# Kernel optimization log

Hardware: AMD Instinct MI355X
Metric: run time of the kernel (lower is better)

Reference implementation:

```python
import jax, jax.numpy as jnp
import numpy as np

B, S, HID = 2, 2048, 1024
NH, HD = 16, 64  # op_heads, head_size; op_size = NH*HD = 1024


def setup_inputs() -> dict:
    key = jax.random.key(0)
    k1, k2, k3 = jax.random.split(key, 3)
    hidden_states = jax.random.normal(k1, (B, S, HID), dtype=jnp.float32)
    # Linear weights stored as [in, out] for x @ W + b
    Wqk = jax.random.normal(k2, (HID, 2 * NH * HD), dtype=jnp.float32) * (HID ** -0.5)
    bqk = jnp.zeros((2 * NH * HD,), dtype=jnp.float32)
    Wv = jax.random.normal(k3, (HID, NH * HD), dtype=jnp.float32) * (HID ** -0.5)
    bv = jnp.zeros((NH * HD,), dtype=jnp.float32)
    return {"hidden_states": hidden_states, "Wqk": Wqk, "bqk": bqk, "Wv": Wv, "bv": bv}


def _split_heads(t):
    # [B, S, NH*HD] -> [B, NH, S, HD]
    b, s, _ = t.shape
    return t.reshape(b, s, NH, HD).transpose(0, 2, 1, 3)


def reference(hidden_states, Wqk, bqk, Wv, bv):
    op_size = NH * HD
    qk = hidden_states @ Wqk + bqk                      # [B, S, 2*op_size]
    query, key = qk[..., :op_size], qk[..., op_size:]
    value = hidden_states @ Wv + bv                     # [B, S, op_size]
    q = _split_heads(query)                             # [B, H, S, D]
    k = _split_heads(key)
    v = _split_heads(value)
    # scores: [B, H, Sq, Sk], scaled by sqrt(head_dim) (scale_attn_weights=True)
    scores = jnp.einsum('bhqd,bhkd->bhqk', q, k) / jnp.asarray(HD ** 0.5, q.dtype)
    s = scores.shape[-1]
    causal = jnp.tril(jnp.ones((s, s), dtype=bool))     # [S, S]
    mask_value = jnp.finfo(scores.dtype).min
    scores = jnp.where(causal, scores, mask_value)
    attn = jax.nn.softmax(scores, axis=-1)              # dropout is identity (eval)
    out = jnp.einsum('bhqk,bhkd->bhqd', attn, v)        # [B, H, S, D]
    out = out.transpose(0, 2, 1, 3).reshape(out.shape[0], out.shape[2], NH * HD)
    return out
```

## Files before the change

kernel.cpp:

```cpp
#include <hip/hip_runtime.h>

typedef float floatx4 __attribute__((ext_vector_type(4)));
typedef float floatx16 __attribute__((ext_vector_type(16)));
typedef __bf16 bf16x8 __attribute__((ext_vector_type(8)));
typedef unsigned short u16x8 __attribute__((ext_vector_type(8)));
typedef unsigned short u16x4 __attribute__((ext_vector_type(4)));

#define GLDS16(g, l) __builtin_amdgcn_global_load_lds( \
    (__attribute__((address_space(1))) void*)(g), \
    (__attribute__((address_space(3))) void*)(l), 16, 0, 0)

__device__ __forceinline__ unsigned short f2bf(float f) {
    unsigned u = __float_as_uint(f);
    u += 0x7fffu + ((u >> 16) & 1u);
    return (unsigned short)(u >> 16);
}

#if __has_builtin(__builtin_amdgcn_cvt_pk_bf16_f32)
__device__ __forceinline__ unsigned pk2(float a, float b) {
    typedef __bf16 bf16x2 __attribute__((ext_vector_type(2)));
    union { bf16x2 v; unsigned u; } cv;
    cv.v = __builtin_amdgcn_cvt_pk_bf16_f32(a, b);
    return cv.u;
}
#else
__device__ __forceinline__ unsigned pk2(float a, float b) {
    return (unsigned)f2bf(a) | ((unsigned)f2bf(b) << 16);
}
#endif

#if __has_builtin(__builtin_amdgcn_exp2f)
__device__ __forceinline__ float fast_exp2(float x) { return __builtin_amdgcn_exp2f(x); }
#else
__device__ __forceinline__ float fast_exp2(float x) { return __exp2f(x); }
#endif

__global__ __launch_bounds__(256) void k_prep(const float* __restrict__ hidden,
                                              const float* __restrict__ Wqk,
                                              const float* __restrict__ Wv,
                                              unsigned short* __restrict__ Abf,
                                              unsigned short* __restrict__ Wt) {
    __shared__ unsigned short t[64][68];
    const int tid = threadIdx.x;
    if (blockIdx.x < 2048) {
        int idx = (blockIdx.x * 256 + tid) * 8;
        const float4* p = (const float4*)(hidden + idx);
        float4 f0 = p[0], f1 = p[1];
        u16x8 o;
        o[0] = f2bf(f0.x); o[1] = f2bf(f0.y); o[2] = f2bf(f0.z); o[3] = f2bf(f0.w);
        o[4] = f2bf(f1.x); o[5] = f2bf(f1.y); o[6] = f2bf(f1.z); o[7] = f2bf(f1.w);
        *(u16x8*)(Abf + idx) = o;
        return;
    }
    const int bx = blockIdx.x - 2048;
    const int n0 = (bx % 48) * 64;
    const int k0 = (bx / 48) * 64;
    const int nl = tid & 63;
    const int kb = tid >> 6;
    const int ng = n0 + nl;
#pragma unroll
    for (int i = 0; i < 16; ++i) {
        int kl = kb + i * 4;
        float v = (n0 < 2048) ? Wqk[(size_t)(k0 + kl) * 2048 + ng]
                              : Wv[(size_t)(k0 + kl) * 1024 + (ng - 2048)];
        t[nl][kl] = f2bf(v);
    }
    __syncthreads();
    const int k4 = (tid & 15) * 4;
    const int nb = tid >> 4;
#pragma unroll
    for (int i = 0; i < 4; ++i) {
        int n2 = nb + i * 16;
        u16x4 o;
        o[0] = t[n2][k4]; o[1] = t[n2][k4 + 1]; o[2] = t[n2][k4 + 2]; o[3] = t[n2][k4 + 3];
        *(u16x4*)(Wt + (size_t)(n0 + n2) * 1024 + k0 + k4) = o;
    }
}

__global__ __launch_bounds__(256, 3) void k_gemm_qkv(
    const unsigned short* __restrict__ A,
    const unsigned short* __restrict__ Bt,
    const float* __restrict__ bqk, const float* __restrict__ bvv,
    unsigned short* __restrict__ Qf, unsigned short* __restrict__ Kf,
    unsigned short* __restrict__ Vf) {
    __shared__ unsigned short As[2][128 * 32];
    __shared__ unsigned short Bs[2][128 * 32];
    const int tid = threadIdx.x;
    const int lane = tid & 63;
    const int w = tid >> 6;
    const int l15 = lane & 15;
    const int quad = lane >> 4;
    const int gb = blockIdx.x;
    const int q = gb >> 3;
    const int m0 = ((((gb & 7) << 2) | (q & 3))) * 128;
    const int n0 = (q >> 2) * 128;
    const bool isV = (n0 >= 2048);
    const int wm = (w & 1) * 64;
    const int wn = (w >> 1) * 64;
    const int rC = lane >> 2;
    const int kC = (lane & 3) * 8;
    const int c0 = w * 2;

    floatx4 acc[4][4] = {};

    const unsigned short* agp0 = A + (size_t)(m0 + c0 * 16 + rC) * 1024 + kC;
    const unsigned short* agp1 = agp0 + 16 * 1024;
    const unsigned short* bgp0 = Bt + (size_t)(n0 + c0 * 16 + rC) * 1024 + kC;
    const unsigned short* bgp1 = bgp0 + 16 * 1024;

    for (int k0 = 0; k0 < 1024; k0 += 64) {
#pragma unroll
        for (int h = 0; h < 2; ++h) {
            GLDS16(agp0 + k0 + h * 32, &As[h][c0 * 512]);
            GLDS16(agp1 + k0 + h * 32, &As[h][c0 * 512 + 512]);
            GLDS16(bgp0 + k0 + h * 32, &Bs[h][c0 * 512]);
            GLDS16(bgp1 + k0 + h * 32, &Bs[h][c0 * 512 + 512]);
        }
        __syncthreads();
#pragma unroll
        for (int h = 0; h < 2; ++h) {
            const unsigned short* ap = &As[h][(wm + l15) * 32 + quad * 8];
            const unsigned short* bp = &Bs[h][(wn + l15) * 32 + quad * 8];
            bf16x8 af[4], bfr[4];
#pragma unroll
            for (int mi = 0; mi < 4; ++mi) af[mi] = *(const bf16x8*)(ap + mi * 16 * 32);
#pragma unroll
            for (int ni = 0; ni < 4; ++ni) bfr[ni] = *(const bf16x8*)(bp + ni * 16 * 32);
            if (!isV) {
#pragma unroll
                for (int mi = 0; mi < 4; ++mi)
#pragma unroll
                    for (int ni = 0; ni < 4; ++ni)
                        acc[mi][ni] = __builtin_amdgcn_mfma_f32_16x16x32_bf16(bfr[ni], af[mi],
                                                                              acc[mi][ni], 0, 0, 0);
            } else {
#pragma unroll
                for (int mi = 0; mi < 4; ++mi)
#pragma unroll
                    for (int ni = 0; ni < 4; ++ni)
                        acc[mi][ni] = __builtin_amdgcn_mfma_f32_16x16x32_bf16(af[mi], bfr[ni],
                                                                              acc[mi][ni], 0, 0, 0);
            }
        }
        __syncthreads();
    }
    if (!isV) {
        const bool isQ = (n0 < 1024);
        unsigned short* dst = isQ ? Qf : Kf;
        const float scale = isQ ? 0.18033688011112042f : 1.0f;
#pragma unroll
        for (int mi = 0; mi < 4; ++mi) {
            const int m = m0 + wm + mi * 16 + l15;
            const int b = m >> 11, s = m & 2047;
            const int t = s >> 5, cc = s & 31;
#pragma unroll
            for (int ni = 0; ni < 4; ++ni) {
                const int nb = n0 + wn + ni * 16 + (quad << 2);
                const float4 bq = *(const float4*)(bqk + nb);
                const int hd = isQ ? nb : nb - 1024;
                const int h = hd >> 6, d = hd & 63;
                const int kb = d >> 4, hhd = (d >> 3) & 1, jj = d & 7;
                const int bh = b * 16 + h;
                u16x4 o4;
                o4[0] = f2bf((acc[mi][ni][0] + bq.x) * scale);
                o4[1] = f2bf((acc[mi][ni][1] + bq.y) * scale);
                o4[2] = f2bf((acc[mi][ni][2] + bq.z) * scale);
                o4[3] = f2bf((acc[mi][ni][3] + bq.w) * scale);
                size_t idx = ((((size_t)(bh * 64 + t) * 4 + kb) * 2 + hhd) * 32 + cc) * 8 + jj;
                *(u16x4*)(dst + idx) = o4;
            }
        }
    } else {
#pragma unroll
        for (int ni = 0; ni < 4; ++ni) {
            const int n = n0 + wn + ni * 16 + l15;
            const float bias = bvv[n - 2048];
            const int hd = n - 2048;
            const int h = hd >> 6, d = hd & 63;
            const int dt = d >> 5, cc = d & 31;
#pragma unroll
            for (int mi = 0; mi < 4; ++mi) {
                const int m = m0 + wm + mi * 16 + (quad << 2);
                const int b = m >> 11, s = m & 2047;
                const int bh = b * 16 + h, t = s >> 5, kvr = s & 31;
                const int mb = kvr >> 4, hhv = (kvr >> 3) & 1, jj0 = s & 7;
                u16x4 o4;
#pragma unroll
                for (int r = 0; r < 4; ++r) o4[r] = f2bf(acc[mi][ni][r] + bias);
                size_t idx = (((((size_t)(bh * 64 + t) * 2 + mb) * 2 + dt) * 2 + hhv) * 32 + cc) * 8 + jj0;
                *(u16x4*)(Vf + idx) = o4;
            }
        }
    }
}

__global__ __launch_bounds__(256, 3) void k_attn(
    const unsigned short* __restrict__ Qf, const unsigned short* __restrict__ Kf,
    const unsigned short* __restrict__ Vf, float* __restrict__ out,
    float* __restrict__ Op1, float* __restrict__ l0, float* __restrict__ l1) {
    const int tid = threadIdx.x;
    const int lane = tid & 63;
    const int w = tid >> 6;
    const int c = lane & 31;
    const int hh = lane >> 5;
    const int gb = blockIdx.x;
    const int xcd = gb & 7;
    const int idx = gb >> 3;
    const int bh = xcd + ((idx & 3) << 3);
    const int u = idx >> 2;
    int a, mode;
    if (u < 8) { a = 8 + u; mode = 1; }
    else {
        const int i = u - 8;
        if ((i & 1) == 0) { a = 7 - (i >> 1); mode = 0; }
        else              { a = 15 - (i >> 1); mode = 2; }
    }
    const int j = 4 * a + w;
    const int t0 = (mode == 2) ? 32 : 0;
    const int t1 = (mode == 1) ? 31 : j;
    const int q_abs = j * 32 + c;

    bf16x8 qf[4];
    {
        const unsigned short* qp = Qf + (size_t)(bh * 64 + j) * 2048 + lane * 8;
#pragma unroll
        for (int kb = 0; kb < 4; ++kb) qf[kb] = *(const bf16x8*)(qp + kb * 512);
    }
    const unsigned short* kbase = Kf + (size_t)bh * (64 * 2048) + lane * 8;
    const unsigned short* vbase = Vf + (size_t)bh * (64 * 2048) + lane * 8;

    floatx16 o2[2] = {};
    float ls0 = 0.f, ls1 = 0.f;

    bf16x8 kf[4];
    {
        const unsigned short* kp = kbase + (size_t)t0 * 2048;
#pragma unroll
        for (int kb = 0; kb < 4; ++kb) kf[kb] = *(const bf16x8*)(kp + kb * 512);
    }

    for (int t = t0; t <= t1; ++t) {
        const unsigned short* vp = vbase + (size_t)t * 2048;
        bf16x8 vf[4];
#pragma unroll
        for (int f = 0; f < 4; ++f) vf[f] = *(const bf16x8*)(vp + f * 512);

        floatx16 st = {};
#pragma unroll
        for (int kb = 0; kb < 4; ++kb)
            st = __builtin_amdgcn_mfma_f32_32x32x16_bf16(kf[kb], qf[kb], st, 0, 0, 0);

        bf16x8 kn[4];
        if (t < t1) {
            const unsigned short* kpn = kbase + (size_t)(t + 1) * 2048;
#pragma unroll
            for (int kb = 0; kb < 4; ++kb) kn[kb] = *(const bf16x8*)(kpn + kb * 512);
        }

        if (t == j) {
#pragma unroll
            for (int i = 0; i < 16; ++i) {
                const int kvr = (i & 3) + 8 * (i >> 2) + 4 * hh;
                if (kvr > c) st[i] = -1e30f;
            }
        }

        float a0 = 0.f, a1 = 0.f, a2 = 0.f, a3 = 0.f;
#pragma unroll
        for (int i = 0; i < 16; i += 4) {
            float p0 = fast_exp2(st[i + 0]);
            float p1 = fast_exp2(st[i + 1]);
            float p2 = fast_exp2(st[i + 2]);
            float p3 = fast_exp2(st[i + 3]);
            st[i + 0] = p0; st[i + 1] = p1; st[i + 2] = p2; st[i + 3] = p3;
            a0 += p0; a1 += p1; a2 += p2; a3 += p3;
        }
        ls0 += a0 + a2; ls1 += a1 + a3;

#pragma unroll
        for (int mb = 0; mb < 2; ++mb) {
            const int rb = mb * 8;
            unsigned p0 = pk2(st[rb + 0], st[rb + 1]);
            unsigned p1 = pk2(st[rb + 2], st[rb + 3]);
            unsigned p2 = pk2(st[rb + 4], st[rb + 5]);
            unsigned p3 = pk2(st[rb + 6], st[rb + 7]);
            unsigned sA = hh ? p0 : p2;
            unsigned sB = hh ? p1 : p3;
            unsigned rA = (unsigned)__shfl_xor((int)sA, 32, 64);
            unsigned rB = (unsigned)__shfl_xor((int)sB, 32, 64);
            union { unsigned u4[4]; bf16x8 v; } pf;
            if (hh == 0) { pf.u4[0] = p0; pf.u4[1] = p1; pf.u4[2] = rA; pf.u4[3] = rB; }
            else         { pf.u4[0] = rA; pf.u4[1] = rB; pf.u4[2] = p2; pf.u4[3] = p3; }
#pragma unroll
            for (int dt = 0; dt < 2; ++dt)
                o2[dt] = __builtin_amdgcn_mfma_f32_32x32x16_bf16(vf[mb * 2 + dt], pf.v,
                                                                 o2[dt], 0, 0, 0);
        }
#pragma unroll
        for (int kb = 0; kb < 4; ++kb) kf[kb] = kn[kb];
    }

    const int b = bh >> 4, head = bh & 15;
    float lrow = ls0 + ls1;
    lrow += __shfl_xor(lrow, 32, 64);
    if (mode == 0) {
        const float inv = 1.0f / lrow;
        float* op = out + (size_t)(b * 2048 + q_abs) * 1024 + head * 64;
#pragma unroll
        for (int dt = 0; dt < 2; ++dt)
#pragma unroll
            for (int rr = 0; rr < 4; ++rr) {
                float4 v4 = make_float4(o2[dt][rr * 4 + 0] * inv, o2[dt][rr * 4 + 1] * inv,
                                        o2[dt][rr * 4 + 2] * inv, o2[dt][rr * 4 + 3] * inv);
                *(float4*)(op + dt * 32 + rr * 8 + hh * 4) = v4;
            }
    } else {
        const int qr = q_abs - 1024;
        float* op;
        if (mode == 1) {
            if (hh == 0) l0[bh * 1024 + qr] = lrow;
            op = out + (size_t)(b * 2048 + q_abs) * 1024 + head * 64;
        } else {
            if (hh == 0) l1[bh * 1024 + qr] = lrow;
            op = Op1 + (size_t)(bh * 1024 + qr) * 64;
        }
#pragma unroll
        for (int dt = 0; dt < 2; ++dt)
#pragma unroll
            for (int rr = 0; rr < 4; ++rr) {
                float4 v4 = make_float4(o2[dt][rr * 4 + 0], o2[dt][rr * 4 + 1],
                                        o2[dt][rr * 4 + 2], o2[dt][rr * 4 + 3]);
                *(float4*)(op + dt * 32 + rr * 8 + hh * 4) = v4;
            }
    }
}

__global__ __launch_bounds__(256) void k_comb(const float* __restrict__ Op1,
                                              const float* __restrict__ l0,
                                              const float* __restrict__ l1,
                                              float* __restrict__ out) {
    const int idx = blockIdx.x * 256 + threadIdx.x;
    const int bh = idx >> 14;
    const int rem = idx & 16383;
    const int qr = rem >> 4;
    const int d4 = (rem & 15) << 2;
    const float inv = 1.0f / (l0[bh * 1024 + qr] + l1[bh * 1024 + qr]);
    const int b = bh >> 4, h = bh & 15;
    float* op = out + (size_t)(b * 2048 + 1024 + qr) * 1024 + h * 64 + d4;
    const float* pp = Op1 + (size_t)(bh * 1024 + qr) * 64 + d4;
    float4 a = *(const float4*)op;
    float4 p = *(const float4*)pp;
    float4 r = make_float4((a.x + p.x) * inv, (a.y + p.y) * inv,
                           (a.z + p.z) * inv, (a.w + p.w) * inv);
    *(float4*)op = r;
}

extern "C" void kernel_launch(void* const* d_in, const int* in_sizes, int n_in,
                              void* d_out, int out_size, void* d_ws, size_t ws_size,
                              hipStream_t stream) {
    const float* hidden = (const float*)d_in[0];
    const float* Wqk    = (const float*)d_in[1];
    const float* bqk    = (const float*)d_in[2];
    const float* Wv     = (const float*)d_in[3];
    const float* bvv    = (const float*)d_in[4];
    float* out = (float*)d_out;

    unsigned short* Abf = (unsigned short*)d_ws;
    unsigned short* Wt  = Abf + 4096 * 1024;
    unsigned short* Qf  = Wt + 3072 * 1024;
    unsigned short* Kf  = Qf + 32 * 2048 * 64;
    unsigned short* Vf  = Kf + 32 * 2048 * 64;
    float* Op1 = (float*)d_ws;
    float* l0  = Op1 + 32 * 1024 * 64;
    float* l1  = l0 + 32 * 1024;

    k_prep<<<2816, 256, 0, stream>>>(hidden, Wqk, Wv, Abf, Wt);
    k_gemm_qkv<<<768, 256, 0, stream>>>(Abf, Wt, bqk, bvv, Qf, Kf, Vf);
    k_attn<<<768, 256, 0, stream>>>(Qf, Kf, Vf, out, Op1, l0, l1);
    k_comb<<<2048, 256, 0, stream>>>(Op1, l0, l1, out);
}
```

Measured before the change: 160.3 us.

## Pre-pack GEMM operands into MFMA fragment layout and load directly to registers

The prep kernel now writes the bf16 activations and transposed weights in a fragment-tiled layout, with 16-row by 32-k tiles of 64 lanes times 8 values, that matches the MFMA operand order. The QKV GEMM then drops its LDS staging and barriers and reads fragments straight from global memory into registers, with a one-step register prefetch. This removes the LDS traffic and the synchronisation from the GEMM. In exchange, each wave reads its own A and B fragments from global or L2 with no sharing through LDS, so global load traffic goes up and latency hiding depends on a single k-step prefetch.

```diff
diff --git a/kernel.cpp b/kernel.cpp
--- a/kernel.cpp
+++ b/kernel.cpp
@@ -5,10 +5,6 @@
 typedef __bf16 bf16x8 __attribute__((ext_vector_type(8)));
 typedef unsigned short u16x8 __attribute__((ext_vector_type(8)));
 typedef unsigned short u16x4 __attribute__((ext_vector_type(4)));
-
-#define GLDS16(g, l) __builtin_amdgcn_global_load_lds( \
-    (__attribute__((address_space(1))) void*)(g), \
-    (__attribute__((address_space(3))) void*)(l), 16, 0, 0)
 
 __device__ __forceinline__ unsigned short f2bf(float f) {
     unsigned u = __float_as_uint(f);
@@ -38,21 +34,32 @@
 __global__ __launch_bounds__(256) void k_prep(const float* __restrict__ hidden,
                                               const float* __restrict__ Wqk,
                                               const float* __restrict__ Wv,
-                                              unsigned short* __restrict__ Abf,
-                                              unsigned short* __restrict__ Wt) {
+                                              unsigned short* __restrict__ Af,
+                                              unsigned short* __restrict__ Wtf) {
     __shared__ unsigned short t[64][68];
     const int tid = threadIdx.x;
-    if (blockIdx.x < 2048) {
-        int idx = (blockIdx.x * 256 + tid) * 8;
-        const float4* p = (const float4*)(hidden + idx);
-        float4 f0 = p[0], f1 = p[1];
-        u16x8 o;
-        o[0] = f2bf(f0.x); o[1] = f2bf(f0.y); o[2] = f2bf(f0.z); o[3] = f2bf(f0.w);
-        o[4] = f2bf(f1.x); o[5] = f2bf(f1.y); o[6] = f2bf(f1.z); o[7] = f2bf(f1.w);
-        *(u16x8*)(Abf + idx) = o;
+    const int lane = tid & 63;
+    const int w = tid >> 6;
+    const int l15 = lane & 15;
+    const int quad = lane >> 4;
+    if (blockIdx.x < 512) {
+        const int mt = blockIdx.x >> 1;
+        const int half = blockIdx.x & 1;
+        const int m0 = mt * 16;
+#pragma unroll
+        for (int r = 0; r < 4; ++r) {
+            const int kc = half * 16 + r * 4 + w;
+            const float* src = hidden + (size_t)(m0 + l15) * 1024 + kc * 32 + quad * 8;
+            float4 a = *(const float4*)src;
+            float4 b = *(const float4*)(src + 4);
+            u16x8 o;
+            o[0] = f2bf(a.x); o[1] = f2bf(a.y); o[2] = f2bf(a.z); o[3] = f2bf(a.w);
+            o[4] = f2bf(b.x); o[5] = f2bf(b.y); o[6] = f2bf(b.z); o[7] = f2bf(b.w);
+            *(u16x8*)(Af + ((size_t)(mt * 32 + kc) * 64 + lane) * 8) = o;
+        }
         return;
     }
-    const int bx = blockIdx.x - 2048;
+    const int bx = blockIdx.x - 512;
     const int n0 = (bx % 48) * 64;
     const int k0 = (bx / 48) * 64;
     const int nl = tid & 63;
@@ -66,25 +73,29 @@
         t[nl][kl] = f2bf(v);
     }
     __syncthreads();
-    const int k4 = (tid & 15) * 4;
-    const int nb = tid >> 4;
-#pragma unroll
-    for (int i = 0; i < 4; ++i) {
-        int n2 = nb + i * 16;
-        u16x4 o;
-        o[0] = t[n2][k4]; o[1] = t[n2][k4 + 1]; o[2] = t[n2][k4 + 2]; o[3] = t[n2][k4 + 3];
-        *(u16x4*)(Wt + (size_t)(n0 + n2) * 1024 + k0 + k4) = o;
+#pragma unroll
+    for (int pi = 0; pi < 2; ++pi) {
+        const int p = tid + pi * 256;
+        const int ntl = p >> 7;
+        const int kcl = (p >> 6) & 1;
+        const int lo = p & 63;
+        const int nloc = ntl * 16 + (lo & 15);
+        const int kloc = kcl * 32 + (lo >> 4) * 8;
+        u16x8 o;
+#pragma unroll
+        for (int j = 0; j < 8; ++j) o[j] = t[nloc][kloc + j];
+        const int nt_g = (n0 >> 4) + ntl;
+        const int kc_g = (k0 >> 5) + kcl;
+        *(u16x8*)(Wtf + ((size_t)(nt_g * 32 + kc_g) * 64 + lo) * 8) = o;
     }
 }
 
 __global__ __launch_bounds__(256, 3) void k_gemm_qkv(
-    const unsigned short* __restrict__ A,
-    const unsigned short* __restrict__ Bt,
+    const unsigned short* __restrict__ Af,
+    const unsigned short* __restrict__ Wtf,
     const float* __restrict__ bqk, const float* __restrict__ bvv,
     unsigned short* __restrict__ Qf, unsigned short* __restrict__ Kf,
     unsigned short* __restrict__ Vf) {
-    __shared__ unsigned short As[2][128 * 32];
-    __shared__ unsigned short Bs[2][128 * 32];
     const int tid = threadIdx.x;
     const int lane = tid & 63;
     const int w = tid >> 6;
@@ -97,53 +108,46 @@
     const bool isV = (n0 >= 2048);
     const int wm = (w & 1) * 64;
     const int wn = (w >> 1) * 64;
-    const int rC = lane >> 2;
-    const int kC = (lane & 3) * 8;
-    const int c0 = w * 2;
+
+    const unsigned short* Ab = Af  + ((size_t)((m0 >> 4) + (w & 1) * 4) * 32) * 512 + lane * 8;
+    const unsigned short* Bb = Wtf + ((size_t)((n0 >> 4) + (w >> 1) * 4) * 32) * 512 + lane * 8;
 
     floatx4 acc[4][4] = {};
-
-    const unsigned short* agp0 = A + (size_t)(m0 + c0 * 16 + rC) * 1024 + kC;
-    const unsigned short* agp1 = agp0 + 16 * 1024;
-    const unsigned short* bgp0 = Bt + (size_t)(n0 + c0 * 16 + rC) * 1024 + kC;
-    const unsigned short* bgp1 = bgp0 + 16 * 1024;
-
-    for (int k0 = 0; k0 < 1024; k0 += 64) {
-#pragma unroll
-        for (int h = 0; h < 2; ++h) {
-            GLDS16(agp0 + k0 + h * 32, &As[h][c0 * 512]);
-            GLDS16(agp1 + k0 + h * 32, &As[h][c0 * 512 + 512]);
-            GLDS16(bgp0 + k0 + h * 32, &Bs[h][c0 * 512]);
-            GLDS16(bgp1 + k0 + h * 32, &Bs[h][c0 * 512 + 512]);
-        }
-        __syncthreads();
-#pragma unroll
-        for (int h = 0; h < 2; ++h) {
-            const unsigned short* ap = &As[h][(wm + l15) * 32 + quad * 8];
-            const unsigned short* bp = &Bs[h][(wn + l15) * 32 + quad * 8];
-            bf16x8 af[4], bfr[4];
-#pragma unroll
-            for (int mi = 0; mi < 4; ++mi) af[mi] = *(const bf16x8*)(ap + mi * 16 * 32);
-#pragma unroll
-            for (int ni = 0; ni < 4; ++ni) bfr[ni] = *(const bf16x8*)(bp + ni * 16 * 32);
-            if (!isV) {
-#pragma unroll
-                for (int mi = 0; mi < 4; ++mi)
-#pragma unroll
-                    for (int ni = 0; ni < 4; ++ni)
-                        acc[mi][ni] = __builtin_amdgcn_mfma_f32_16x16x32_bf16(bfr[ni], af[mi],
-                                                                              acc[mi][ni], 0, 0, 0);
-            } else {
-#pragma unroll
-                for (int mi = 0; mi < 4; ++mi)
-#pragma unroll
-                    for (int ni = 0; ni < 4; ++ni)
-                        acc[mi][ni] = __builtin_amdgcn_mfma_f32_16x16x32_bf16(af[mi], bfr[ni],
-                                                                              acc[mi][ni], 0, 0, 0);
-            }
-        }
-        __syncthreads();
-    }
+    bf16x8 af[4], bfr[4];
+#pragma unroll
+    for (int i = 0; i < 4; ++i) {
+        af[i]  = *(const bf16x8*)(Ab + (size_t)(i * 32) * 512);
+        bfr[i] = *(const bf16x8*)(Bb + (size_t)(i * 32) * 512);
+    }
+
+    for (int kc = 0; kc < 32; ++kc) {
+        bf16x8 an[4], bn[4];
+        if (kc < 31) {
+#pragma unroll
+            for (int i = 0; i < 4; ++i) {
+                an[i] = *(const bf16x8*)(Ab + (size_t)(i * 32 + kc + 1) * 512);
+                bn[i] = *(const bf16x8*)(Bb + (size_t)(i * 32 + kc + 1) * 512);
+            }
+        }
+        if (!isV) {
+#pragma unroll
+            for (int mi = 0; mi < 4; ++mi)
+#pragma unroll
+                for (int ni = 0; ni < 4; ++ni)
+                    acc[mi][ni] = __builtin_amdgcn_mfma_f32_16x16x32_bf16(bfr[ni], af[mi],
+                                                                          acc[mi][ni], 0, 0, 0);
+        } else {
+#pragma unroll
+            for (int mi = 0; mi < 4; ++mi)
+#pragma unroll
+                for (int ni = 0; ni < 4; ++ni)
+                    acc[mi][ni] = __builtin_amdgcn_mfma_f32_16x16x32_bf16(af[mi], bfr[ni],
+                                                                          acc[mi][ni], 0, 0, 0);
+        }
+#pragma unroll
+        for (int i = 0; i < 4; ++i) { af[i] = an[i]; bfr[i] = bn[i]; }
+    }
+
     if (!isV) {
         const bool isQ = (n0 < 1024);
         unsigned short* dst = isQ ? Qf : Kf;
@@ -365,17 +369,17 @@
     const float* bvv    = (const float*)d_in[4];
     float* out = (float*)d_out;
 
-    unsigned short* Abf = (unsigned short*)d_ws;
-    unsigned short* Wt  = Abf + 4096 * 1024;
-    unsigned short* Qf  = Wt + 3072 * 1024;
+    unsigned short* Af  = (unsigned short*)d_ws;
+    unsigned short* Wtf = Af + 4096 * 1024;
+    unsigned short* Qf  = Wtf + 3072 * 1024;
     unsigned short* Kf  = Qf + 32 * 2048 * 64;
     unsigned short* Vf  = Kf + 32 * 2048 * 64;
     float* Op1 = (float*)d_ws;
     float* l0  = Op1 + 32 * 1024 * 64;
     float* l1  = l0 + 32 * 1024;
 
-    k_prep<<<2816, 256, 0, stream>>>(hidden, Wqk, Wv, Abf, Wt);
-    k_gemm_qkv<<<768, 256, 0, stream>>>(Abf, Wt, bqk, bvv, Qf, Kf, Vf);
+    k_prep<<<1280, 256, 0, stream>>>(hidden, Wqk, Wv, Af, Wtf);
+    k_gemm_qkv<<<768, 256, 0, stream>>>(Af, Wtf, bqk, bvv, Qf, Kf, Vf);
     k_attn<<<768, 256, 0, stream>>>(Qf, Kf, Vf, out, Op1, l0, l1);
     k_comb<<<2048, 256, 0, stream>>>(Op1, l0, l1, out);
 }
```

After: 151.0 us. -5.8%, faster.
